# Kernel optimization log

Hardware: AMD Instinct MI355X
Metric: run time of the kernel (lower is better)

The kernel has to match this reference:

```python
import jax, jax.numpy as jnp
import numpy as np

TEMPERATURE = 0.7
REDUCTION = "mean"
MARGIN = 0.5  # the '+0.5' shift inside exp in the original


def setup_inputs() -> dict:
    key = jax.random.key(0)
    k1, k2 = jax.random.split(key)
    projection = jax.random.normal(k1, (8192, 256), dtype=jnp.float32)
    y = jax.random.randint(k2, (8192,), 0, 10, dtype=jnp.int64)
    return {"projection": projection, "y": y}


def reference(projection, y):
    # L2-normalize rows, cosine similarity matrix [n, n]
    n = projection.shape[0]
    proj = projection / jnp.linalg.norm(projection, axis=1, keepdims=True)
    sim = proj @ proj.T

    eq = (y[:, None] == y[None, :]).astype(sim.dtype)
    same = eq - jnp.eye(n, dtype=sim.dtype)   # same class, excluding self
    diff = 1.0 - eq                            # different class

    # Original per-row loop computes log(1 + sum_{j in diff, k in same}
    #   exp((sim[i,j] - sim[i,k] + 0.5)/t)) which separates as
    #   exp(0.5/t) * (sum_j exp(sim[i,j]/t)) * (sum_k exp(-sim[i,k]/t)).
    # Empty set -> the loop substitutes [0], i.e. that factor becomes exp(0)=1.
    A = jnp.sum(diff * jnp.exp(sim / TEMPERATURE), axis=1)
    B = jnp.sum(same * jnp.exp(-sim / TEMPERATURE), axis=1)
    A = jnp.where(jnp.sum(diff, axis=1) > 0, A, 1.0)
    B = jnp.where(jnp.sum(same, axis=1) > 0, B, 1.0)

    loss_per_row = jnp.log1p(jnp.exp(MARGIN / TEMPERATURE) * A * B)
    if REDUCTION == "mean":
        return jnp.mean(loss_per_row)
    return jnp.sum(loss_per_row)
```

## Files before the change

### kernel.cpp

```cpp
#include <hip/hip_runtime.h>
#include <hip/hip_bf16.h>


#define NF 256
#define TINV (1.0f / 0.7f)
#define SC2 2.0609929398439434f

typedef __attribute__((ext_vector_type(8))) short short8;
typedef __attribute__((ext_vector_type(4))) float float4v;

typedef const __attribute__((address_space(1))) unsigned int glb_u32;
typedef __attribute__((address_space(3))) unsigned int lds_u32;

__global__ __launch_bounds__(256)
void k_prep(const float* __restrict__ P, unsigned short* __restrict__ Pn,
            float* __restrict__ AB, float* __restrict__ out) {
    int wave = threadIdx.x >> 6, lane = threadIdx.x & 63;
    int row = blockIdx.x * 4 + wave;
    if (threadIdx.x < 8) AB[blockIdx.x * 8 + threadIdx.x] = 0.f;
    if (blockIdx.x == 0 && threadIdx.x == 0) out[0] = 0.f;
    float4 v = *(const float4*)(P + (size_t)row * NF + lane * 4);
    float sq = v.x * v.x + v.y * v.y + v.z * v.z + v.w * v.w;
#pragma unroll
    for (int off = 32; off; off >>= 1) sq += __shfl_xor(sq, off, 64);
    float r = rsqrtf(sq);
    __hip_bfloat16 h0 = __float2bfloat16(v.x * r), h1 = __float2bfloat16(v.y * r),
                   h2 = __float2bfloat16(v.z * r), h3 = __float2bfloat16(v.w * r);
    ushort4 o = { *(unsigned short*)&h0, *(unsigned short*)&h1,
                  *(unsigned short*)&h2, *(unsigned short*)&h3 };
    *(ushort4*)(Pn + (size_t)row * NF + lane * 4) = o;
}

__global__ __launch_bounds__(256, 2)
void k_main(const unsigned short* __restrict__ Pn, const int* __restrict__ y,
            float* __restrict__ Aacc, float* __restrict__ Bacc,
            float* __restrict__ colPart) {
    __shared__ __align__(16) unsigned short Bs[64 * NF];
    __shared__ int yc[128];
    __shared__ float colA[128], colB[128];

    const int tid = threadIdx.x;
    int bid = blockIdx.x;
    int C2 = (int)((sqrtf(8.0f * (float)bid + 1.0f) - 1.0f) * 0.5f);
    while ((C2 * (C2 + 1)) / 2 > bid) --C2;
    while (((C2 + 1) * (C2 + 2)) / 2 <= bid) ++C2;
    const int I = bid - (C2 * (C2 + 1)) / 2;
    const int rb = I * 128, cb0 = C2 * 128;
    const bool offdiag = (I < C2);

    const int lane = tid & 63, wave = tid >> 6;
    const int quad = lane >> 4, l15 = lane & 15;

#define DMA_CHUNK(c)                                                          \
    {                                                                         \
        _Pragma("unroll")                                                     \
        for (int i = 0; i < 8; ++i) {                                         \
            const int kc = wave * 8 + i;                                      \
            const unsigned short* src =                                       \
                Pn + (size_t)(cb0 + (c) * 64 + lane) * NF + kc * 8;           \
            __builtin_amdgcn_global_load_lds((glb_u32*)src,                   \
                (lds_u32*)&Bs[kc * 512], 16, 0, 0);                           \
        }                                                                     \
    }

    DMA_CHUNK(0)

    if (tid < 128) {
        yc[tid] = y[cb0 + tid];
        colA[tid] = 0.f;
        colB[tid] = 0.f;
    }

    const unsigned short* pa = Pn + (size_t)(rb + wave * 32 + l15) * NF + quad * 8;
    short8 afr[2][8];
#pragma unroll
    for (int tr = 0; tr < 2; ++tr)
#pragma unroll
        for (int ks = 0; ks < 8; ++ks)
            afr[tr][ks] = *(const short8*)(pa + (size_t)tr * 16 * NF + ks * 32);

    unsigned yis[2];
#pragma unroll
    for (int tr = 0; tr < 2; ++tr) {
        int4 v = *(const int4*)(y + rb + wave * 32 + tr * 16 + quad * 4);
        yis[tr] = (unsigned)(v.x & 255) | ((unsigned)(v.y & 255) << 8) |
                  ((unsigned)(v.z & 255) << 16) | ((unsigned)(v.w & 255) << 24);
    }

    float rA[2][4], rB[2][4];
#pragma unroll
    for (int tr = 0; tr < 2; ++tr)
#pragma unroll
        for (int r = 0; r < 4; ++r) { rA[tr][r] = 0.f; rB[tr][r] = 0.f; }

#pragma unroll 1
    for (int c = 0; c < 2; ++c) {
        __syncthreads();

        float4v acc[2][4];
#pragma unroll
        for (int a = 0; a < 2; ++a)
#pragma unroll
            for (int b = 0; b < 4; ++b) acc[a][b] = (float4v){0.f, 0.f, 0.f, 0.f};

#pragma unroll
        for (int ks = 0; ks < 8; ++ks) {
            short8 fb[4];
#pragma unroll
            for (int tc = 0; tc < 4; ++tc)
                fb[tc] = *(const short8*)&Bs[(ks * 4 + quad) * 512 + (tc * 16 + l15) * 8];
#pragma unroll
            for (int tr = 0; tr < 2; ++tr)
#pragma unroll
                for (int tc = 0; tc < 4; ++tc)
                    acc[tr][tc] = __builtin_amdgcn_mfma_f32_16x16x32_bf16(
                        afr[tr][ks], fb[tc], acc[tr][tc], 0, 0, 0);
        }
        __syncthreads();
        if (c < 1) DMA_CHUNK(1)

        if (offdiag) {
#pragma unroll
            for (int tc = 0; tc < 4; ++tc) {
                const int jl = c * 64 + tc * 16 + l15;
                const int yj = yc[jl];
                float ca = 0.f, cb = 0.f;
#pragma unroll
                for (int tr = 0; tr < 2; ++tr)
#pragma unroll
                    for (int r = 0; r < 4; ++r) {
                        const float s = acc[tr][tc][r];
                        const int cls = (yis[tr] >> (8 * r)) & 255;
                        const bool same = (cls == yj);
                        const float e = exp2f(s * (same ? -SC2 : SC2));
                        rA[tr][r] += same ? 0.f : e;
                        rB[tr][r] += same ? e : 0.f;
                        ca += same ? 0.f : e;
                        cb += same ? e : 0.f;
                    }
                ca += __shfl_xor(ca, 16, 64); ca += __shfl_xor(ca, 32, 64);
                cb += __shfl_xor(cb, 16, 64); cb += __shfl_xor(cb, 32, 64);
                if (quad == 0) {
                    atomicAdd(&colA[jl], ca);
                    atomicAdd(&colB[jl], cb);
                }
            }
        } else {
#pragma unroll
            for (int tc = 0; tc < 4; ++tc) {
                const int jl = c * 64 + tc * 16 + l15;
                const int yj = yc[jl];
                const int gj = cb0 + jl;
#pragma unroll
                for (int tr = 0; tr < 2; ++tr) {
                    const int gi0 = rb + wave * 32 + tr * 16 + quad * 4;
#pragma unroll
                    for (int r = 0; r < 4; ++r) {
                        const float s = acc[tr][tc][r];
                        const int cls = (yis[tr] >> (8 * r)) & 255;
                        const bool same = (cls == yj);
                        const float e = exp2f(s * (same ? -SC2 : SC2));
                        rA[tr][r] += same ? 0.f : e;
                        rB[tr][r] += (same && (gi0 + r != gj)) ? e : 0.f;
                    }
                }
            }
        }
    }

#pragma unroll
    for (int tr = 0; tr < 2; ++tr)
#pragma unroll
        for (int r = 0; r < 4; ++r) {
#pragma unroll
            for (int off = 1; off < 16; off <<= 1) {
                rA[tr][r] += __shfl_xor(rA[tr][r], off, 64);
                rB[tr][r] += __shfl_xor(rB[tr][r], off, 64);
            }
        }
    if (l15 == 0) {
#pragma unroll
        for (int tr = 0; tr < 2; ++tr)
#pragma unroll
            for (int r = 0; r < 4; ++r) {
                const int gi = rb + wave * 32 + tr * 16 + quad * 4 + r;
                atomicAdd(&Aacc[gi], rA[tr][r]);
                atomicAdd(&Bacc[gi], rB[tr][r]);
            }
    }

    if (offdiag) {
        __syncthreads();
        float* cp = colPart + (size_t)bid * 256;
        cp[tid] = (tid < 128) ? colA[tid] : colB[tid - 128];
    }
}

__global__ __launch_bounds__(256)
void k_tail(const float* __restrict__ colPart, const float* __restrict__ Aacc,
            const float* __restrict__ Bacc, const int* __restrict__ y,
            float* __restrict__ out, int n) {
    __shared__ int hist[16];
    __shared__ float red[4];
    const int tid = threadIdx.x;
    if (tid < 16) hist[tid] = 0;
    __syncthreads();
    int loc[10];
#pragma unroll
    for (int cc = 0; cc < 10; ++cc) loc[cc] = 0;
    for (int i = tid; i < n; i += 256) {
        const int yv = y[i];
#pragma unroll
        for (int cc = 0; cc < 10; ++cc) {
            unsigned long long m = __ballot(yv == cc);
            if ((tid & 63) == 0) loc[cc] += __popcll(m);
        }
    }
    if ((tid & 63) == 0)
#pragma unroll
        for (int cc = 0; cc < 10; ++cc) atomicAdd(&hist[cc], loc[cc]);
    __syncthreads();

    const int jloc = tid >> 1, half = tid & 1;
    const int j = blockIdx.x * 128 + jloc;
    const int C2 = j >> 7, o = j & 127;
    const float* p = colPart + ((size_t)(C2 * (C2 + 1)) / 2 + half) * 256 + o;
    float sA = 0.f, sB = 0.f;
    for (int I = half; I < C2; I += 2) {
        sA += p[0];
        sB += p[128];
        p += 512;
    }
    sA += __shfl_xor(sA, 1, 64);
    sB += __shfl_xor(sB, 1, 64);

    float term = 0.f;
    if (half == 0) {
        const float M = __expf(0.5f * TINV);
        const int cc = hist[y[j] & 15];
        float a = Aacc[j] + sA;
        float b = Bacc[j] + sB;
        a = (n - cc) > 0 ? a : 1.0f;
        b = (cc - 1) > 0 ? b : 1.0f;
        term = log1pf(M * a * b);
    }
#pragma unroll
    for (int off = 32; off; off >>= 1) term += __shfl_xor(term, off, 64);
    if ((tid & 63) == 0) red[tid >> 6] = term;
    __syncthreads();
    if (tid == 0)
        atomicAdd(out, (red[0] + red[1] + red[2] + red[3]) / (float)n);
}

extern "C" void kernel_launch(void* const* d_in, const int* in_sizes, int n_in,
                              void* d_out, int out_size, void* d_ws, size_t ws_size,
                              hipStream_t stream) {
    const float* P = (const float*)d_in[0];
    const int* y   = (const int*)d_in[1];
    float* out     = (float*)d_out;
    const int n = in_sizes[1];

    unsigned short* Pn = (unsigned short*)d_ws;
    float* Aacc = (float*)((char*)d_ws + (size_t)n * NF * 2);
    float* Bacc = Aacc + n;
    float* colPart = Bacc + n;

    const int np = n / 128;
    const int nblk = np * (np + 1) / 2;
    k_prep<<<n / 4, 256, 0, stream>>>(P, Pn, Aacc, out);
    k_main<<<nblk, 256, 0, stream>>>(Pn, y, Aacc, Bacc, colPart);
    k_tail<<<n / 128, 256, 0, stream>>>(colPart, Aacc, Bacc, y, out, n);
}
```

Baseline: 141.6 us.

## Use 512-thread blocks with one 16-row tile per wave and both B chunks preloaded

Doubles the waves per 128x128 tile from 4 to 8, so each wave handles a single 16-row MFMA strip instead of two. LDS now holds both 64-column B chunks, and both are loaded by async DMA at kernel start, which removes the mid-loop barrier and reload. The goal is more waves to hide latency and lower register pressure per wave. In exchange LDS use per block doubles to 64KB, which may limit resident blocks per CU, and each wave gets less MFMA reuse of B fragments.

```diff
diff --git a/kernel.cpp b/kernel.cpp
--- a/kernel.cpp
+++ b/kernel.cpp
@@ -31,11 +31,11 @@
     *(ushort4*)(Pn + (size_t)row * NF + lane * 4) = o;
 }
 
-__global__ __launch_bounds__(256, 2)
+__global__ __launch_bounds__(512, 4)
 void k_main(const unsigned short* __restrict__ Pn, const int* __restrict__ y,
             float* __restrict__ Aacc, float* __restrict__ Bacc,
             float* __restrict__ colPart) {
-    __shared__ __align__(16) unsigned short Bs[64 * NF];
+    __shared__ __align__(16) unsigned short Bs[2][32 * 512];
     __shared__ int yc[128];
     __shared__ float colA[128], colB[128];
 
@@ -54,16 +54,17 @@
 #define DMA_CHUNK(c)                                                          \
     {                                                                         \
         _Pragma("unroll")                                                     \
-        for (int i = 0; i < 8; ++i) {                                         \
-            const int kc = wave * 8 + i;                                      \
+        for (int i = 0; i < 4; ++i) {                                         \
+            const int kc = wave * 4 + i;                                      \
             const unsigned short* src =                                       \
                 Pn + (size_t)(cb0 + (c) * 64 + lane) * NF + kc * 8;           \
             __builtin_amdgcn_global_load_lds((glb_u32*)src,                   \
-                (lds_u32*)&Bs[kc * 512], 16, 0, 0);                           \
+                (lds_u32*)&Bs[c][kc * 512], 16, 0, 0);                        \
         }                                                                     \
     }
 
     DMA_CHUNK(0)
+    DMA_CHUNK(1)
 
     if (tid < 128) {
         yc[tid] = y[cb0 + tid];
@@ -71,53 +72,42 @@
         colB[tid] = 0.f;
     }
 
-    const unsigned short* pa = Pn + (size_t)(rb + wave * 32 + l15) * NF + quad * 8;
-    short8 afr[2][8];
-#pragma unroll
-    for (int tr = 0; tr < 2; ++tr)
-#pragma unroll
-        for (int ks = 0; ks < 8; ++ks)
-            afr[tr][ks] = *(const short8*)(pa + (size_t)tr * 16 * NF + ks * 32);
-
-    unsigned yis[2];
-#pragma unroll
-    for (int tr = 0; tr < 2; ++tr) {
-        int4 v = *(const int4*)(y + rb + wave * 32 + tr * 16 + quad * 4);
-        yis[tr] = (unsigned)(v.x & 255) | ((unsigned)(v.y & 255) << 8) |
-                  ((unsigned)(v.z & 255) << 16) | ((unsigned)(v.w & 255) << 24);
-    }
-
-    float rA[2][4], rB[2][4];
-#pragma unroll
-    for (int tr = 0; tr < 2; ++tr)
-#pragma unroll
-        for (int r = 0; r < 4; ++r) { rA[tr][r] = 0.f; rB[tr][r] = 0.f; }
+    const unsigned short* pa = Pn + (size_t)(rb + wave * 16 + l15) * NF + quad * 8;
+    short8 afr[8];
+#pragma unroll
+    for (int ks = 0; ks < 8; ++ks)
+        afr[ks] = *(const short8*)(pa + ks * 32);
+
+    unsigned yis;
+    {
+        int4 v = *(const int4*)(y + rb + wave * 16 + quad * 4);
+        yis = (unsigned)(v.x & 255) | ((unsigned)(v.y & 255) << 8) |
+              ((unsigned)(v.z & 255) << 16) | ((unsigned)(v.w & 255) << 24);
+    }
+
+    float rA[4], rB[4];
+#pragma unroll
+    for (int r = 0; r < 4; ++r) { rA[r] = 0.f; rB[r] = 0.f; }
+
+    __syncthreads();
 
 #pragma unroll 1
     for (int c = 0; c < 2; ++c) {
-        __syncthreads();
-
-        float4v acc[2][4];
-#pragma unroll
-        for (int a = 0; a < 2; ++a)
-#pragma unroll
-            for (int b = 0; b < 4; ++b) acc[a][b] = (float4v){0.f, 0.f, 0.f, 0.f};
+        float4v acc[4];
+#pragma unroll
+        for (int b = 0; b < 4; ++b) acc[b] = (float4v){0.f, 0.f, 0.f, 0.f};
 
 #pragma unroll
         for (int ks = 0; ks < 8; ++ks) {
             short8 fb[4];
 #pragma unroll
             for (int tc = 0; tc < 4; ++tc)
-                fb[tc] = *(const short8*)&Bs[(ks * 4 + quad) * 512 + (tc * 16 + l15) * 8];
-#pragma unroll
-            for (int tr = 0; tr < 2; ++tr)
-#pragma unroll
-                for (int tc = 0; tc < 4; ++tc)
-                    acc[tr][tc] = __builtin_amdgcn_mfma_f32_16x16x32_bf16(
-                        afr[tr][ks], fb[tc], acc[tr][tc], 0, 0, 0);
-        }
-        __syncthreads();
-        if (c < 1) DMA_CHUNK(1)
+                fb[tc] = *(const short8*)&Bs[c][(ks * 4 + quad) * 512 + (tc * 16 + l15) * 8];
+#pragma unroll
+            for (int tc = 0; tc < 4; ++tc)
+                acc[tc] = __builtin_amdgcn_mfma_f32_16x16x32_bf16(
+                    afr[ks], fb[tc], acc[tc], 0, 0, 0);
+        }
 
         if (offdiag) {
 #pragma unroll
@@ -126,18 +116,16 @@
                 const int yj = yc[jl];
                 float ca = 0.f, cb = 0.f;
 #pragma unroll
-                for (int tr = 0; tr < 2; ++tr)
-#pragma unroll
-                    for (int r = 0; r < 4; ++r) {
-                        const float s = acc[tr][tc][r];
-                        const int cls = (yis[tr] >> (8 * r)) & 255;
-                        const bool same = (cls == yj);
-                        const float e = exp2f(s * (same ? -SC2 : SC2));
-                        rA[tr][r] += same ? 0.f : e;
-                        rB[tr][r] += same ? e : 0.f;
-                        ca += same ? 0.f : e;
-                        cb += same ? e : 0.f;
-                    }
+                for (int r = 0; r < 4; ++r) {
+                    const float s = acc[tc][r];
+                    const int cls = (yis >> (8 * r)) & 255;
+                    const bool same = (cls == yj);
+                    const float e = exp2f(s * (same ? -SC2 : SC2));
+                    rA[r] += same ? 0.f : e;
+                    rB[r] += same ? e : 0.f;
+                    ca += same ? 0.f : e;
+                    cb += same ? e : 0.f;
+                }
                 ca += __shfl_xor(ca, 16, 64); ca += __shfl_xor(ca, 32, 64);
                 cb += __shfl_xor(cb, 16, 64); cb += __shfl_xor(cb, 32, 64);
                 if (quad == 0) {
@@ -151,48 +139,43 @@
                 const int jl = c * 64 + tc * 16 + l15;
                 const int yj = yc[jl];
                 const int gj = cb0 + jl;
-#pragma unroll
-                for (int tr = 0; tr < 2; ++tr) {
-                    const int gi0 = rb + wave * 32 + tr * 16 + quad * 4;
-#pragma unroll
-                    for (int r = 0; r < 4; ++r) {
-                        const float s = acc[tr][tc][r];
-                        const int cls = (yis[tr] >> (8 * r)) & 255;
-                        const bool same = (cls == yj);
-                        const float e = exp2f(s * (same ? -SC2 : SC2));
-                        rA[tr][r] += same ? 0.f : e;
-                        rB[tr][r] += (same && (gi0 + r != gj)) ? e : 0.f;
-                    }
+                const int gi0 = rb + wave * 16 + quad * 4;
+#pragma unroll
+                for (int r = 0; r < 4; ++r) {
+                    const float s = acc[tc][r];
+                    const int cls = (yis >> (8 * r)) & 255;
+                    const bool same = (cls == yj);
+                    const float e = exp2f(s * (same ? -SC2 : SC2));
+                    rA[r] += same ? 0.f : e;
+                    rB[r] += (same && (gi0 + r != gj)) ? e : 0.f;
                 }
             }
         }
     }
 
 #pragma unroll
-    for (int tr = 0; tr < 2; ++tr)
+    for (int r = 0; r < 4; ++r) {
+#pragma unroll
+        for (int off = 1; off < 16; off <<= 1) {
+            rA[r] += __shfl_xor(rA[r], off, 64);
+            rB[r] += __shfl_xor(rB[r], off, 64);
+        }
+    }
+    if (l15 == 0) {
 #pragma unroll
         for (int r = 0; r < 4; ++r) {
-#pragma unroll
-            for (int off = 1; off < 16; off <<= 1) {
-                rA[tr][r] += __shfl_xor(rA[tr][r], off, 64);
-                rB[tr][r] += __shfl_xor(rB[tr][r], off, 64);
-            }
-        }
-    if (l15 == 0) {
-#pragma unroll
-        for (int tr = 0; tr < 2; ++tr)
-#pragma unroll
-            for (int r = 0; r < 4; ++r) {
-                const int gi = rb + wave * 32 + tr * 16 + quad * 4 + r;
-                atomicAdd(&Aacc[gi], rA[tr][r]);
-                atomicAdd(&Bacc[gi], rB[tr][r]);
-            }
+            const int gi = rb + wave * 16 + quad * 4 + r;
+            atomicAdd(&Aacc[gi], rA[r]);
+            atomicAdd(&Bacc[gi], rB[r]);
+        }
     }
 
     if (offdiag) {
         __syncthreads();
-        float* cp = colPart + (size_t)bid * 256;
-        cp[tid] = (tid < 128) ? colA[tid] : colB[tid - 128];
+        if (tid < 256) {
+            float* cp = colPart + (size_t)bid * 256;
+            cp[tid] = (tid < 128) ? colA[tid] : colB[tid - 128];
+        }
     }
 }
 
@@ -268,6 +251,6 @@
     const int np = n / 128;
     const int nblk = np * (np + 1) / 2;
     k_prep<<<n / 4, 256, 0, stream>>>(P, Pn, Aacc, out);
-    k_main<<<nblk, 256, 0, stream>>>(Pn, y, Aacc, Bacc, colPart);
+    k_main<<<nblk, 512, 0, stream>>>(Pn, y, Aacc, Bacc, colPart);
     k_tail<<<n / 128, 256, 0, stream>>>(colPart, Aacc, Bacc, y, out, n);
 }
```

Measured after the change: 139.0 us. No clear change (-1.8%).
